# Kernel optimization log

Hardware: AMD Instinct MI355X
Metric: run time of the kernel (lower is better)

Reference implementation:

```python
import jax, jax.numpy as jnp
import numpy as np

N = 50000      # nodes
E = 800000     # edges
F = 128        # num_features == emb_dim
K = 8          # latent factors
d = 16         # emb_dim // K
G = 512        # num graphs
GC = 3         # gc_layers = num_layer - head_layers = 5 - 2
BN_EPS = 1e-5


def setup_inputs() -> dict:
    key = jax.random.key(0)
    ks = jax.random.split(key, 24)
    x = jax.random.normal(ks[0], (N, F), jnp.float32)
    edge_index = jax.random.randint(ks[1], (2, E), 0, N, jnp.int32)
    batch = jnp.sort(jax.random.randint(ks[2], (N,), 0, G, jnp.int32))
    s = 0.05
    inp = {
        'x': x, 'edge_index': edge_index, 'batch': batch, 'num_graphs': G,
        # stacked gc-layer GIN MLP params (all [F,F] since num_features==emb_dim)
        'gc_W1': jax.random.normal(ks[3], (GC, F, F), jnp.float32) * s,
        'gc_b1': jnp.zeros((GC, F), jnp.float32),
        'gc_W2': jax.random.normal(ks[4], (GC, F, F), jnp.float32) * s,
        'gc_b2': jnp.zeros((GC, F), jnp.float32),
        'gc_g': jnp.ones((GC, F), jnp.float32),
        'gc_be': jnp.zeros((GC, F), jnp.float32),
        # disentangled head layer 0 (per factor k): Linear(F,d), Linear(d,d)
        'h0_W1': jax.random.normal(ks[5], (K, F, d), jnp.float32) * s,
        'h0_b1': jnp.zeros((K, d), jnp.float32),
        'h0_W2': jax.random.normal(ks[6], (K, d, d), jnp.float32) * s,
        'h0_b2': jnp.zeros((K, d), jnp.float32),
        'h0_g': jnp.ones((K, d), jnp.float32),
        'h0_be': jnp.zeros((K, d), jnp.float32),
        # disentangled head layer 1: Linear(d,d), Linear(d,d)
        'h1_W1': jax.random.normal(ks[7], (K, d, d), jnp.float32) * s,
        'h1_b1': jnp.zeros((K, d), jnp.float32),
        'h1_W2': jax.random.normal(ks[8], (K, d, d), jnp.float32) * s,
        'h1_b2': jnp.zeros((K, d), jnp.float32),
        'h1_g': jnp.ones((K, d), jnp.float32),
        'h1_be': jnp.zeros((K, d), jnp.float32),
    }
    return inp


def _gin(h, src, dst, W1, b1, W2, b2):
    # GINConv(eps=0): nn(x + sum_{j in N(i)} x_j)
    agg = jax.ops.segment_sum(h[src], dst, num_segments=N)
    z = h + agg
    return jax.nn.relu(z @ W1 + b1) @ W2 + b2


def _bn(z, g, be):
    # BatchNorm1d, training-mode batch statistics over the node axis
    mu = jnp.mean(z, axis=0)
    var = jnp.var(z, axis=0)
    return (z - mu) * jax.lax.rsqrt(var + BN_EPS) * g + be


def reference(x, edge_index, batch, num_graphs,
              gc_W1, gc_b1, gc_W2, gc_b2, gc_g, gc_be,
              h0_W1, h0_b1, h0_W2, h0_b2, h0_g, h0_be,
              h1_W1, h1_b1, h1_W2, h1_b2, h1_g, h1_be):
    src, dst = edge_index[0], edge_index[1]
    # _normal_conv (JK='last', drop_ratio=0, residual off)
    h = x
    for i in range(GC):
        h = _gin(h, src, dst, gc_W1[i], gc_b1[i], gc_W2[i], gc_b2[i])
        h = _bn(h, gc_g[i], gc_be[i])
        if i < GC - 1:
            h = jax.nn.relu(h)
    # _disen_conv: K factor heads, head_layers=2, vmapped over K
    def head(W1a, b1a, W2a, b2a, ga, bea, W1b, b1b, W2b, b2b, gb, beb):
        z = _gin(h, src, dst, W1a, b1a, W2a, b2a)
        z = jax.nn.relu(_bn(z, ga, bea))
        z = _gin(z, src, dst, W1b, b1b, W2b, b2b)
        return _bn(z, gb, beb)
    x_node = jax.vmap(head)(h0_W1, h0_b1, h0_W2, h0_b2, h0_g, h0_be,
                            h1_W1, h1_b1, h1_W2, h1_b2, h1_g, h1_be)  # [K,N,d]
    # global_add_pool per factor
    pool = jax.vmap(lambda z: jax.ops.segment_sum(z, batch, num_segments=num_graphs))
    x_graph = pool(x_node)                        # [K,G,d]
    z_graph = jnp.transpose(x_graph, (1, 0, 2))   # [G,K,d]
    return z_graph
```

## Files before the change

### kernel.cpp

```cpp
#include <hip/hip_runtime.h>

#define NN 50000
#define NE 800000
#define FF 128
#define KF 8
#define DD 16
#define GG 512
#define BN_EPS 1e-5f
#define NB 196
#define KSTR 264
#define BSTR 20

using s8v = __attribute__((ext_vector_type(8))) short;
using f4v = __attribute__((ext_vector_type(4))) float;
using h4v = __attribute__((ext_vector_type(4))) _Float16;
using h8v = __attribute__((ext_vector_type(8))) _Float16;
typedef unsigned int u32;

__device__ __forceinline__ void gload_lds16(const void* g, void* l) {
    __builtin_amdgcn_global_load_lds((const __attribute__((address_space(1))) u32*)g,
                                     (__attribute__((address_space(3))) u32*)l, 16, 0, 0);
}

__global__ void k_deg(const int* __restrict__ dst, int* __restrict__ deg) {
    int e = blockIdx.x * 256 + threadIdx.x;
    if (e < NE) atomicAdd(&deg[dst[e]], 1);
}

__global__ __launch_bounds__(256) void k_bsum(const int* __restrict__ deg, int* __restrict__ bsum) {
    int idx = blockIdx.x * 256 + threadIdx.x;
    int v = (idx < NN) ? deg[idx] : 0;
#pragma unroll
    for (int off = 32; off; off >>= 1) v += __shfl_down(v, off, 64);
    __shared__ int ws[4];
    if ((threadIdx.x & 63) == 0) ws[threadIdx.x >> 6] = v;
    __syncthreads();
    if (threadIdx.x == 0) bsum[blockIdx.x] = ws[0] + ws[1] + ws[2] + ws[3];
}

__global__ __launch_bounds__(256) void k_bscan(const int* __restrict__ bsum, int* __restrict__ boffs) {
    __shared__ int s[256];
    int tid = threadIdx.x;
    int v = (tid < NB) ? bsum[tid] : 0;
    s[tid] = v;
    __syncthreads();
    for (int off = 1; off < 256; off <<= 1) {
        int t = (tid >= off) ? s[tid - off] : 0;
        __syncthreads();
        s[tid] += t;
        __syncthreads();
    }
    if (tid < NB) boffs[tid] = s[tid] - v;
}

__global__ __launch_bounds__(256) void k_offs(const int* __restrict__ deg,
                                              const int* __restrict__ boffs,
                                              int* __restrict__ offs) {
    __shared__ int s[256];
    int tid = threadIdx.x;
    int idx = blockIdx.x * 256 + tid;
    int v = (idx < NN) ? deg[idx] : 0;
    s[tid] = v;
    __syncthreads();
    for (int off = 1; off < 256; off <<= 1) {
        int t = (tid >= off) ? s[tid - off] : 0;
        __syncthreads();
        s[tid] += t;
        __syncthreads();
    }
    int incl = s[tid];
    if (idx < NN) offs[idx] = boffs[blockIdx.x] + incl - v;
    if (idx == NN - 1) offs[NN] = boffs[blockIdx.x] + incl;
}

__global__ void k_fill(const int* __restrict__ src, const int* __restrict__ dst,
                       const int* __restrict__ offs, int* __restrict__ cnt,
                       int* __restrict__ csr) {
    int e = blockIdx.x * 256 + threadIdx.x;
    if (e < NE) {
        int d = dst[e];
        int p = atomicAdd(&cnt[d], 1);
        csr[offs[d] + p] = src[e];
    }
}

__device__ __forceinline__ void bn_coefs(const float* st, const float* g, const float* be,
                                         int lane, float4& a4, float4& b4) {
    const float inv_n = 1.0f / (float)NN;
    float av[4], bv[4];
#pragma unroll
    for (int t = 0; t < 4; t++) {
        int c = lane * 4 + t;
        float mu = st[c] * inv_n;
        float var = st[FF + c] * inv_n - mu * mu;
        float a = g[c] * rsqrtf(var + BN_EPS);
        av[t] = a;
        bv[t] = be[c] - mu * a;
    }
    a4 = make_float4(av[0], av[1], av[2], av[3]);
    b4 = make_float4(bv[0], bv[1], bv[2], bv[3]);
}

__device__ __forceinline__ float4 h2f(h4v h) {
    return make_float4((float)h.x, (float)h.y, (float)h.z, (float)h.w);
}

__global__ __launch_bounds__(256) void k_cvt(const float4* __restrict__ X, h4v* __restrict__ O) {
    int i = blockIdx.x * 256 + threadIdx.x;
    if (i < NN * 32) {
        float4 v = X[i];
        h4v o;
        o.x = (_Float16)v.x; o.y = (_Float16)v.y;
        o.z = (_Float16)v.z; o.w = (_Float16)v.w;
        O[i] = o;
    }
}

__global__ __launch_bounds__(256) void k_wprep(const float* __restrict__ W1,
                                               const float* __restrict__ W2,
                                               unsigned short* __restrict__ out) {
    int idx = blockIdx.x * 256 + threadIdx.x;
    if (idx >= 3 * 2 * 16384) return;
    int l = idx / (2 * 16384);
    int rem = idx % (2 * 16384);
    int mat = rem >> 14;
    int e = rem & 16383;
    int n = e >> 7, k = e & 127;
    const float* W = (mat == 0) ? (W1 + (size_t)l * 16384) : (W2 + (size_t)l * 16384);
    float v = W[k * 128 + n];
    _Float16* o = (_Float16*)out + (size_t)(l * 2 + mat) * 16384;
    o[n * 128 + k] = (_Float16)v;
}

__global__ __launch_bounds__(256) void k_wprep_h0(const float* __restrict__ W1,
                                                  const float* __restrict__ W2,
                                                  unsigned short* __restrict__ out) {
    int idx = blockIdx.x * 256 + threadIdx.x;
    if (idx >= 2 * 16384) return;
    int mat = idx >> 14;
    int e = idx & 16383;
    int n = e >> 7, k = e & 127;
    float v;
    if (mat == 0) {
        v = W1[(n >> 4) * (FF * DD) + k * DD + (n & 15)];
    } else {
        v = ((k >> 4) == (n >> 4)) ? W2[(n >> 4) * 256 + (k & 15) * DD + (n & 15)] : 0.f;
    }
    _Float16* o = (_Float16*)out + (size_t)(6 + mat) * 16384;
    o[n * 128 + k] = (_Float16)v;
}

template <bool BN, bool RELU>
__global__ __launch_bounds__(256) void k_agg(const h4v* __restrict__ X,
                                             const int* __restrict__ offs,
                                             const int* __restrict__ csr,
                                             const float* __restrict__ st,
                                             const float* __restrict__ g,
                                             const float* __restrict__ be,
                                             h4v* __restrict__ Zh) {
    int grp = threadIdx.x >> 5;
    int lane = threadIdx.x & 31;
    int n = blockIdx.x * 8 + grp;

    float4 a4 = make_float4(1.f, 1.f, 1.f, 1.f);
    float4 b4 = make_float4(0.f, 0.f, 0.f, 0.f);
    if (BN) bn_coefs(st, g, be, lane, a4, b4);

    auto apply = [&](float4 v) -> float4 {
        if (BN) {
            v.x = fmaf(v.x, a4.x, b4.x);
            v.y = fmaf(v.y, a4.y, b4.y);
            v.z = fmaf(v.z, a4.z, b4.z);
            v.w = fmaf(v.w, a4.w, b4.w);
        }
        if (RELU) {
            v.x = fmaxf(v.x, 0.f);
            v.y = fmaxf(v.y, 0.f);
            v.z = fmaxf(v.z, 0.f);
            v.w = fmaxf(v.w, 0.f);
        }
        return v;
    };
    auto add4 = [](float4& a, float4 b) {
        a.x += b.x; a.y += b.y; a.z += b.z; a.w += b.w;
    };

    float4 acc = apply(h2f(X[(size_t)n * 32 + lane]));
    int e0 = offs[n], e1 = offs[n + 1];
    int e = e0;
    int s0, s1, s2, s3, s4, s5, s6, s7;
    if (e + 8 <= e1) {
        s0 = csr[e]; s1 = csr[e + 1]; s2 = csr[e + 2]; s3 = csr[e + 3];
        s4 = csr[e + 4]; s5 = csr[e + 5]; s6 = csr[e + 6]; s7 = csr[e + 7];
    }
    while (e + 8 <= e1) {
        h4v r0 = X[(size_t)s0 * 32 + lane];
        h4v r1 = X[(size_t)s1 * 32 + lane];
        h4v r2 = X[(size_t)s2 * 32 + lane];
        h4v r3 = X[(size_t)s3 * 32 + lane];
        h4v r4 = X[(size_t)s4 * 32 + lane];
        h4v r5 = X[(size_t)s5 * 32 + lane];
        h4v r6 = X[(size_t)s6 * 32 + lane];
        h4v r7 = X[(size_t)s7 * 32 + lane];
        e += 8;
        int t0 = csr[e], t1 = csr[e + 1], t2 = csr[e + 2], t3 = csr[e + 3];
        int t4 = csr[e + 4], t5 = csr[e + 5], t6 = csr[e + 6], t7 = csr[e + 7];
        float4 v0 = apply(h2f(r0));
        float4 v1 = apply(h2f(r1));
        float4 v2 = apply(h2f(r2));
        float4 v3 = apply(h2f(r3));
        float4 v4 = apply(h2f(r4));
        float4 v5 = apply(h2f(r5));
        float4 v6 = apply(h2f(r6));
        float4 v7 = apply(h2f(r7));
        add4(v0, v1); add4(v2, v3); add4(v4, v5); add4(v6, v7);
        add4(v0, v2); add4(v4, v6); add4(v0, v4); add4(acc, v0);
        s0 = t0; s1 = t1; s2 = t2; s3 = t3;
        s4 = t4; s5 = t5; s6 = t6; s7 = t7;
    }
    for (; e + 4 <= e1; e += 4) {
        int q0 = csr[e], q1 = csr[e + 1], q2 = csr[e + 2], q3 = csr[e + 3];
        float4 v0 = apply(h2f(X[(size_t)q0 * 32 + lane]));
        float4 v1 = apply(h2f(X[(size_t)q1 * 32 + lane]));
        float4 v2 = apply(h2f(X[(size_t)q2 * 32 + lane]));
        float4 v3 = apply(h2f(X[(size_t)q3 * 32 + lane]));
        add4(v0, v1); add4(v2, v3); add4(v0, v2); add4(acc, v0);
    }
    for (; e < e1; e++) {
        float4 v = apply(h2f(X[(size_t)csr[e] * 32 + lane]));
        add4(acc, v);
    }
    h4v o;
    o.x = (_Float16)acc.x; o.y = (_Float16)acc.y;
    o.z = (_Float16)acc.z; o.w = (_Float16)acc.w;
    Zh[(size_t)n * 32 + lane] = o;
}

__global__ __launch_bounds__(256) void gemm_mfma(const _Float16* __restrict__ A,
                                                 const unsigned short* __restrict__ W1T,
                                                 const unsigned short* __restrict__ W2T,
                                                 const float* __restrict__ b1,
                                                 const float* __restrict__ b2,
                                                 _Float16* __restrict__ C,
                                                 float* __restrict__ stout) {
    __shared__ __align__(16) unsigned short Zs[8192];
    __shared__ __align__(16) unsigned short Wch[8192];
    __shared__ float Sred[1024];
    int tid = threadIdx.x;
    int row0 = blockIdx.x * 64;
    int w = tid >> 6, lane = tid & 63, quad = lane >> 4, lid = lane & 15;

    int wsrc[2], wdst[2];
#pragma unroll
    for (int i = 0; i < 2; i++) {
        int L = (w * 2 + i) * 1024 + lane * 16;
        int npair = L >> 7, cc = L & 127;
        int ccp = cc ^ ((npair & 7) << 4);
        wsrc[i] = (npair * 2 + (ccp >> 6)) * 128 + ((ccp & 63) >> 1);
        wdst[i] = (w * 2 + i) * 1024;
    }

#pragma unroll
    for (int i = 0; i < 4; i++) {
        int L = (w * 4 + i) * 1024 + lane * 16;
        int row = L >> 8, cb = L & 255;
        int cbp = cb ^ ((row & 7) << 4);
        int grow = row0 + row;
        if (grow >= NN) grow = NN - 1;
        gload_lds16((const char*)A + (size_t)grow * 256 + cbp,
                    (char*)Zs + (w * 4 + i) * 1024);
    }
#pragma unroll
    for (int i = 0; i < 2; i++)
        gload_lds16(W1T + wsrc[i], (char*)Wch + wdst[i]);
    __syncthreads();

    int lr = w * 16 + lid;
    int swzr = (lr & 7) << 4;
    int abase = lr * 256;
    int boff[8];
#pragma unroll
    for (int n0 = 0; n0 < 8; n0++) {
        int nn = n0 * 16 + lid;
        int cc = ((nn & 1) << 6) | (quad << 4);
        boff[n0] = (nn >> 1) * 128 + (cc ^ (((nn >> 1) & 7) << 4));
    }

    f4v acc[8];
#pragma unroll
    for (int i = 0; i < 8; i++) acc[i] = 0;

    for (int g = 0; g < 8; ++g) {
        int buf = g & 1;
        if (g < 7) {
            const unsigned short* WT = (g + 1 < 4) ? W1T : W2T;
            int kcn = (g + 1) & 3;
#pragma unroll
            for (int i = 0; i < 2; i++)
                gload_lds16(WT + wsrc[i] + kcn * 32,
                            (char*)Wch + (buf ^ 1) * 8192 + wdst[i]);
        }
        int kc = g & 3;
        int aoff = (kc * 64 + quad * 16) ^ swzr;
        h8v a = *(const h8v*)((const char*)Zs + abase + aoff);
        const char* wb = (const char*)Wch + buf * 8192;
#pragma unroll
        for (int n0 = 0; n0 < 8; n0++) {
            h8v b = *(const h8v*)(wb + boff[n0]);
            acc[n0] = __builtin_amdgcn_mfma_f32_16x16x32_f16(a, b, acc[n0], 0, 0, 0);
        }
        if (g == 3) {
#pragma unroll
            for (int n0 = 0; n0 < 8; n0++) {
                int c = n0 * 16 + lid;
                float bb = b1[c];
#pragma unroll
                for (int rr = 0; rr < 4; rr++) {
                    int zr = w * 16 + quad * 4 + rr;
                    float z = fmaxf(acc[n0][rr] + bb, 0.f);
                    int zb = zr * 256 + ((2 * c) ^ ((zr & 7) << 4));
                    *(_Float16*)((char*)Zs + zb) = (_Float16)z;
                }
                acc[n0] = 0;
            }
        }
        if (g < 7) __syncthreads();
    }

#pragma unroll
    for (int n0 = 0; n0 < 8; n0++) {
        int c = n0 * 16 + lid;
        float bb = b2[c];
        float s = 0.f, q = 0.f;
#pragma unroll
        for (int rr = 0; rr < 4; rr++) {
            int grow = row0 + w * 16 + quad * 4 + rr;
            if (grow < NN) {
                float v = acc[n0][rr] + bb;
                C[(size_t)grow * 128 + c] = (_Float16)v;
                s += v;
                q += v * v;
            }
        }
        s += __shfl_xor(s, 16); s += __shfl_xor(s, 32);
        q += __shfl_xor(q, 16); q += __shfl_xor(q, 32);
        if (quad == 0) {
            Sred[w * 128 + c] = s;
            Sred[512 + w * 128 + c] = q;
        }
    }
    __syncthreads();
    if (tid < 128) {
        float s = Sred[tid] + Sred[128 + tid] + Sred[256 + tid] + Sred[384 + tid];
        float q = Sred[512 + tid] + Sred[640 + tid] + Sred[768 + tid] + Sred[896 + tid];
        atomicAdd(&stout[tid], s);
        atomicAdd(&stout[FF + tid], q);
    }
}

__global__ __launch_bounds__(256) void k_aggbd(const h4v* __restrict__ X,
                                               const int* __restrict__ offs,
                                               const int* __restrict__ csr,
                                               const float* __restrict__ st,
                                               const float* __restrict__ g,
                                               const float* __restrict__ be,
                                               const float* __restrict__ W1,
                                               const float4* __restrict__ b1,
                                               const float* __restrict__ W2,
                                               const float4* __restrict__ b2,
                                               float4* __restrict__ C) {
    __shared__ float As[8][8 * BSTR];
    __shared__ float Ts[8][8 * BSTR];
    __shared__ float Ws1[KF * KSTR];
    __shared__ float Ws2[KF * KSTR];
    int grp = threadIdx.x >> 5, lane = threadIdx.x & 31;
    int n = blockIdx.x * 8 + grp;

    for (int l = threadIdx.x; l < KF * 256; l += 256) {
        int k = l >> 8, r = l & 255;
        Ws1[k * KSTR + r] = W1[l];
        Ws2[k * KSTR + r] = W2[l];
    }

    float4 a4, b4;
    bn_coefs(st, g, be, lane, a4, b4);
    auto apply = [&](float4 v) -> float4 {
        v.x = fmaxf(fmaf(v.x, a4.x, b4.x), 0.f);
        v.y = fmaxf(fmaf(v.y, a4.y, b4.y), 0.f);
        v.z = fmaxf(fmaf(v.z, a4.z, b4.z), 0.f);
        v.w = fmaxf(fmaf(v.w, a4.w, b4.w), 0.f);
        return v;
    };
    auto add4 = [](float4& a, float4 b) {
        a.x += b.x; a.y += b.y; a.z += b.z; a.w += b.w;
    };

    float4 acc = apply(h2f(X[(size_t)n * 32 + lane]));
    int e0 = offs[n], e1 = offs[n + 1];
    int e = e0;
    int s0, s1, s2, s3, s4, s5, s6, s7;
    if (e + 8 <= e1) {
        s0 = csr[e]; s1 = csr[e + 1]; s2 = csr[e + 2]; s3 = csr[e + 3];
        s4 = csr[e + 4]; s5 = csr[e + 5]; s6 = csr[e + 6]; s7 = csr[e + 7];
    }
    while (e + 8 <= e1) {
        h4v r0 = X[(size_t)s0 * 32 + lane];
        h4v r1 = X[(size_t)s1 * 32 + lane];
        h4v r2 = X[(size_t)s2 * 32 + lane];
        h4v r3 = X[(size_t)s3 * 32 + lane];
        h4v r4 = X[(size_t)s4 * 32 + lane];
        h4v r5 = X[(size_t)s5 * 32 + lane];
        h4v r6 = X[(size_t)s6 * 32 + lane];
        h4v r7 = X[(size_t)s7 * 32 + lane];
        e += 8;
        int t0 = csr[e], t1 = csr[e + 1], t2 = csr[e + 2], t3 = csr[e + 3];
        int t4 = csr[e + 4], t5 = csr[e + 5], t6 = csr[e + 6], t7 = csr[e + 7];
        float4 v0 = apply(h2f(r0));
        float4 v1 = apply(h2f(r1));
        float4 v2 = apply(h2f(r2));
        float4 v3 = apply(h2f(r3));
        float4 v4 = apply(h2f(r4));
        float4 v5 = apply(h2f(r5));
        float4 v6 = apply(h2f(r6));
        float4 v7 = apply(h2f(r7));
        add4(v0, v1); add4(v2, v3); add4(v4, v5); add4(v6, v7);
        add4(v0, v2); add4(v4, v6); add4(v0, v4); add4(acc, v0);
        s0 = t0; s1 = t1; s2 = t2; s3 = t3;
        s4 = t4; s5 = t5; s6 = t6; s7 = t7;
    }
    for (; e + 4 <= e1; e += 4) {
        int q0 = csr[e], q1 = csr[e + 1], q2 = csr[e + 2], q3 = csr[e + 3];
        float4 v0 = apply(h2f(X[(size_t)q0 * 32 + lane]));
        float4 v1 = apply(h2f(X[(size_t)q1 * 32 + lane]));
        float4 v2 = apply(h2f(X[(size_t)q2 * 32 + lane]));
        float4 v3 = apply(h2f(X[(size_t)q3 * 32 + lane]));
        add4(v0, v1); add4(v2, v3); add4(v0, v2); add4(acc, v0);
    }
    for (; e < e1; e++) {
        float4 v = apply(h2f(X[(size_t)csr[e] * 32 + lane]));
        add4(acc, v);
    }
    *(float4*)&As[grp][(lane >> 2) * BSTR + (lane & 3) * 4] = acc;
    __syncthreads();

    int k = lane >> 2, jb = (lane & 3) * 4;
    float a[16];
    {
        const float4* As4 = (const float4*)&As[grp][k * BSTR];
        float4 a0 = As4[0], a1 = As4[1], a2 = As4[2], a3 = As4[3];
        a[0] = a0.x; a[1] = a0.y; a[2] = a0.z; a[3] = a0.w;
        a[4] = a1.x; a[5] = a1.y; a[6] = a1.z; a[7] = a1.w;
        a[8] = a2.x; a[9] = a2.y; a[10] = a2.z; a[11] = a2.w;
        a[12] = a3.x; a[13] = a3.y; a[14] = a3.z; a[15] = a3.w;
    }
    const float* wp1 = &Ws1[k * KSTR + jb];
    float4 t = b1[lane];
#pragma unroll
    for (int i = 0; i < 16; i++) {
        float4 wv = *(const float4*)&wp1[i * 16];
        t.x = fmaf(a[i], wv.x, t.x);
        t.y = fmaf(a[i], wv.y, t.y);
        t.z = fmaf(a[i], wv.z, t.z);
        t.w = fmaf(a[i], wv.w, t.w);
    }
    t.x = fmaxf(t.x, 0.f); t.y = fmaxf(t.y, 0.f);
    t.z = fmaxf(t.z, 0.f); t.w = fmaxf(t.w, 0.f);
    *(float4*)&Ts[grp][(lane >> 2) * BSTR + (lane & 3) * 4] = t;
    __syncthreads();

    float b[16];
    {
        const float4* Ts4 = (const float4*)&Ts[grp][k * BSTR];
        float4 a0 = Ts4[0], a1 = Ts4[1], a2 = Ts4[2], a3 = Ts4[3];
        b[0] = a0.x; b[1] = a0.y; b[2] = a0.z; b[3] = a0.w;
        b[4] = a1.x; b[5] = a1.y; b[6] = a1.z; b[7] = a1.w;
        b[8] = a2.x; b[9] = a2.y; b[10] = a2.z; b[11] = a2.w;
        b[12] = a3.x; b[13] = a3.y; b[14] = a3.z; b[15] = a3.w;
    }
    const float* wp2 = &Ws2[k * KSTR + jb];
    float4 acc2 = b2[lane];
#pragma unroll
    for (int i = 0; i < 16; i++) {
        float4 wv = *(const float4*)&wp2[i * 16];
        acc2.x = fmaf(b[i], wv.x, acc2.x);
        acc2.y = fmaf(b[i], wv.y, acc2.y);
        acc2.z = fmaf(b[i], wv.z, acc2.z);
        acc2.w = fmaf(b[i], wv.w, acc2.w);
    }
    C[(size_t)n * 32 + lane] = acc2;
}

__global__ __launch_bounds__(256) void k_stats(const float* __restrict__ X,
                                               float* __restrict__ st, int nrows) {
    int c = threadIdx.x & 127;
    int half = threadIdx.x >> 7;
    int rpb = (nrows + gridDim.x - 1) / gridDim.x;
    int r0 = blockIdx.x * rpb;
    int r1 = min(r0 + rpb, nrows);
    float s = 0.f, sq = 0.f;
    for (int r = r0 + half; r < r1; r += 2) {
        float v = X[(size_t)r * FF + c];
        s += v;
        sq += v * v;
    }
    atomicAdd(&st[c], s);
    atomicAdd(&st[FF + c], sq);
}

__global__ __launch_bounds__(128) void k_pool(const float* __restrict__ X,
                                              const int* __restrict__ batch,
                                              const float* __restrict__ st,
                                              const float* __restrict__ g,
                                              const float* __restrict__ be,
                                              float* __restrict__ out) {
    int c = threadIdx.x;
    const float inv_n = 1.0f / (float)NN;
    float mu = st[c] * inv_n;
    float var = st[FF + c] * inv_n - mu * mu;
    float a = g[c] * rsqrtf(var + BN_EPS);
    float b = be[c] - mu * a;
    int chunk = (NN + gridDim.x - 1) / gridDim.x;
    int r0 = blockIdx.x * chunk;
    int r1 = min(r0 + chunk, NN);
    if (r0 >= r1) return;
    float acc = 0.f;
    int cnt = 0;
    int cur = batch[r0];
    for (int r = r0; r < r1; r++) {
        int bb = batch[r];
        if (bb != cur) {
            atomicAdd(&out[(size_t)cur * FF + c], fmaf(a, acc, b * (float)cnt));
            acc = 0.f;
            cnt = 0;
            cur = bb;
        }
        acc += X[(size_t)r * FF + c];
        cnt++;
    }
    atomicAdd(&out[(size_t)cur * FF + c], fmaf(a, acc, b * (float)cnt));
}

extern "C" void kernel_launch(void* const* d_in, const int* in_sizes, int n_in,
                              void* d_out, int out_size, void* d_ws, size_t ws_size,
                              hipStream_t stream) {
    const float* x = (const float*)d_in[0];
    const int* ei = (const int*)d_in[1];
    const int* src = ei;
    const int* dst = ei + NE;
    const int* batch = (const int*)d_in[2];
    const float* gc_W1 = (const float*)d_in[4];
    const float* gc_b1 = (const float*)d_in[5];
    const float* gc_W2 = (const float*)d_in[6];
    const float* gc_b2 = (const float*)d_in[7];
    const float* gc_g = (const float*)d_in[8];
    const float* gc_be = (const float*)d_in[9];
    const float* h0_W1 = (const float*)d_in[10];
    const float* h0_b1 = (const float*)d_in[11];
    const float* h0_W2 = (const float*)d_in[12];
    const float* h0_b2 = (const float*)d_in[13];
    const float* h0_g = (const float*)d_in[14];
    const float* h0_be = (const float*)d_in[15];
    const float* h1_W1 = (const float*)d_in[16];
    const float* h1_b1 = (const float*)d_in[17];
    const float* h1_W2 = (const float*)d_in[18];
    const float* h1_b2 = (const float*)d_in[19];
    const float* h1_g = (const float*)d_in[20];
    const float* h1_be = (const float*)d_in[21];

    const size_t NF = (size_t)NN * FF;
    float* P0 = (float*)d_ws;
    float* P1 = P0 + NF;
    float* P2 = P1 + NF;
    float* stats = P2 + NF;
    int* deg = (int*)(stats + 5 * 256);
    int* cnt = deg + NN;
    int* offs = cnt + NN;
    int* bsum = offs + (NN + 4);
    int* boffs = bsum + 256;
    int* csr = boffs + 256;
    unsigned short* wbf = (unsigned short*)(csr + NE);

    h4v* Zh = (h4v*)P0;
    h4v* Hbuf = (h4v*)P1;

    hipMemsetAsync(deg, 0, (size_t)2 * NN * sizeof(int), stream);
    hipMemsetAsync(stats, 0, 5 * 256 * sizeof(float), stream);
    hipMemsetAsync(d_out, 0, (size_t)GG * KF * DD * sizeof(float), stream);

    k_deg<<<(NE + 255) / 256, 256, 0, stream>>>(dst, deg);
    k_bsum<<<NB, 256, 0, stream>>>(deg, bsum);
    k_bscan<<<1, 256, 0, stream>>>(bsum, boffs);
    k_offs<<<NB, 256, 0, stream>>>(deg, boffs, offs);
    k_fill<<<(NE + 255) / 256, 256, 0, stream>>>(src, dst, offs, cnt, csr);
    k_wprep<<<(3 * 2 * 16384 + 255) / 256, 256, 0, stream>>>(gc_W1, gc_W2, wbf);
    k_wprep_h0<<<(2 * 16384 + 255) / 256, 256, 0, stream>>>(h0_W1, h0_W2, wbf);
    k_cvt<<<(NN * 32 + 255) / 256, 256, 0, stream>>>((const float4*)x, Hbuf);

    const int agg_grid = NN / 8;
    const int gemm_grid = (NN + 63) / 64;

    k_agg<false, false><<<agg_grid, 256, 0, stream>>>(
        Hbuf, offs, csr, nullptr, nullptr, nullptr, Zh);
    gemm_mfma<<<gemm_grid, 256, 0, stream>>>(
        (const _Float16*)Zh, wbf + 0 * 16384, wbf + 1 * 16384, gc_b1, gc_b2,
        (_Float16*)Hbuf, stats);

    k_agg<true, true><<<agg_grid, 256, 0, stream>>>(
        Hbuf, offs, csr, stats, gc_g, gc_be, Zh);
    gemm_mfma<<<gemm_grid, 256, 0, stream>>>(
        (const _Float16*)Zh, wbf + 2 * 16384, wbf + 3 * 16384, gc_b1 + FF, gc_b2 + FF,
        (_Float16*)Hbuf, stats + 256);

    k_agg<true, true><<<agg_grid, 256, 0, stream>>>(
        Hbuf, offs, csr, stats + 256, gc_g + FF, gc_be + FF, Zh);
    gemm_mfma<<<gemm_grid, 256, 0, stream>>>(
        (const _Float16*)Zh, wbf + 4 * 16384, wbf + 5 * 16384, gc_b1 + 2 * FF, gc_b2 + 2 * FF,
        (_Float16*)Hbuf, stats + 512);

    k_agg<true, false><<<agg_grid, 256, 0, stream>>>(
        Hbuf, offs, csr, stats + 512, gc_g + 2 * FF, gc_be + 2 * FF, Zh);
    gemm_mfma<<<gemm_grid, 256, 0, stream>>>(
        (const _Float16*)Zh, wbf + 6 * 16384, wbf + 7 * 16384, h0_b1, h0_b2,
        (_Float16*)Hbuf, stats + 768);

    k_aggbd<<<agg_grid, 256, 0, stream>>>(
        Hbuf, offs, csr, stats + 768, h0_g, h0_be,
        h1_W1, (const float4*)h1_b1, h1_W2, (const float4*)h1_b2, (float4*)P2);
    k_stats<<<256, 256, 0, stream>>>(P2, stats + 1024, NN);

    k_pool<<<512, 128, 0, stream>>>(P2, batch, stats + 1024, h1_g, h1_be, (float*)d_out);
}
```

Before: 576.0 us.

## Fuse neighbor aggregation into MFMA GEMM kernel, writing aggregated rows to LDS

Merges the CSR gather-sum kernel into the MLP GEMM kernel. Each 64-row block first aggregates its nodes' neighbours directly into the swizzled LDS A-tile, which removes the fp16 intermediate write and read and four kernel launches. Buffers now ping-pong so a layer does not overwrite its own input. For the non-ReLU BN case, the affine transform is applied once after summing, scaled by the neighbour count. The risk is lower parallelism in the gather phase: fewer blocks, and each warp half handles 8 nodes serially, so gather latency hiding may drop while the weight load waits behind it.

```diff
diff --git a/kernel.cpp b/kernel.cpp
--- a/kernel.cpp
+++ b/kernel.cpp
@@ -151,92 +151,12 @@
 }
 
 template <bool BN, bool RELU>
-__global__ __launch_bounds__(256) void k_agg(const h4v* __restrict__ X,
-                                             const int* __restrict__ offs,
-                                             const int* __restrict__ csr,
-                                             const float* __restrict__ st,
-                                             const float* __restrict__ g,
-                                             const float* __restrict__ be,
-                                             h4v* __restrict__ Zh) {
-    int grp = threadIdx.x >> 5;
-    int lane = threadIdx.x & 31;
-    int n = blockIdx.x * 8 + grp;
-
-    float4 a4 = make_float4(1.f, 1.f, 1.f, 1.f);
-    float4 b4 = make_float4(0.f, 0.f, 0.f, 0.f);
-    if (BN) bn_coefs(st, g, be, lane, a4, b4);
-
-    auto apply = [&](float4 v) -> float4 {
-        if (BN) {
-            v.x = fmaf(v.x, a4.x, b4.x);
-            v.y = fmaf(v.y, a4.y, b4.y);
-            v.z = fmaf(v.z, a4.z, b4.z);
-            v.w = fmaf(v.w, a4.w, b4.w);
-        }
-        if (RELU) {
-            v.x = fmaxf(v.x, 0.f);
-            v.y = fmaxf(v.y, 0.f);
-            v.z = fmaxf(v.z, 0.f);
-            v.w = fmaxf(v.w, 0.f);
-        }
-        return v;
-    };
-    auto add4 = [](float4& a, float4 b) {
-        a.x += b.x; a.y += b.y; a.z += b.z; a.w += b.w;
-    };
-
-    float4 acc = apply(h2f(X[(size_t)n * 32 + lane]));
-    int e0 = offs[n], e1 = offs[n + 1];
-    int e = e0;
-    int s0, s1, s2, s3, s4, s5, s6, s7;
-    if (e + 8 <= e1) {
-        s0 = csr[e]; s1 = csr[e + 1]; s2 = csr[e + 2]; s3 = csr[e + 3];
-        s4 = csr[e + 4]; s5 = csr[e + 5]; s6 = csr[e + 6]; s7 = csr[e + 7];
-    }
-    while (e + 8 <= e1) {
-        h4v r0 = X[(size_t)s0 * 32 + lane];
-        h4v r1 = X[(size_t)s1 * 32 + lane];
-        h4v r2 = X[(size_t)s2 * 32 + lane];
-        h4v r3 = X[(size_t)s3 * 32 + lane];
-        h4v r4 = X[(size_t)s4 * 32 + lane];
-        h4v r5 = X[(size_t)s5 * 32 + lane];
-        h4v r6 = X[(size_t)s6 * 32 + lane];
-        h4v r7 = X[(size_t)s7 * 32 + lane];
-        e += 8;
-        int t0 = csr[e], t1 = csr[e + 1], t2 = csr[e + 2], t3 = csr[e + 3];
-        int t4 = csr[e + 4], t5 = csr[e + 5], t6 = csr[e + 6], t7 = csr[e + 7];
-        float4 v0 = apply(h2f(r0));
-        float4 v1 = apply(h2f(r1));
-        float4 v2 = apply(h2f(r2));
-        float4 v3 = apply(h2f(r3));
-        float4 v4 = apply(h2f(r4));
-        float4 v5 = apply(h2f(r5));
-        float4 v6 = apply(h2f(r6));
-        float4 v7 = apply(h2f(r7));
-        add4(v0, v1); add4(v2, v3); add4(v4, v5); add4(v6, v7);
-        add4(v0, v2); add4(v4, v6); add4(v0, v4); add4(acc, v0);
-        s0 = t0; s1 = t1; s2 = t2; s3 = t3;
-        s4 = t4; s5 = t5; s6 = t6; s7 = t7;
-    }
-    for (; e + 4 <= e1; e += 4) {
-        int q0 = csr[e], q1 = csr[e + 1], q2 = csr[e + 2], q3 = csr[e + 3];
-        float4 v0 = apply(h2f(X[(size_t)q0 * 32 + lane]));
-        float4 v1 = apply(h2f(X[(size_t)q1 * 32 + lane]));
-        float4 v2 = apply(h2f(X[(size_t)q2 * 32 + lane]));
-        float4 v3 = apply(h2f(X[(size_t)q3 * 32 + lane]));
-        add4(v0, v1); add4(v2, v3); add4(v0, v2); add4(acc, v0);
-    }
-    for (; e < e1; e++) {
-        float4 v = apply(h2f(X[(size_t)csr[e] * 32 + lane]));
-        add4(acc, v);
-    }
-    h4v o;
-    o.x = (_Float16)acc.x; o.y = (_Float16)acc.y;
-    o.z = (_Float16)acc.z; o.w = (_Float16)acc.w;
-    Zh[(size_t)n * 32 + lane] = o;
-}
-
-__global__ __launch_bounds__(256) void gemm_mfma(const _Float16* __restrict__ A,
+__global__ __launch_bounds__(256) void gagg_mfma(const h4v* __restrict__ X,
+                                                 const int* __restrict__ offs,
+                                                 const int* __restrict__ csr,
+                                                 const float* __restrict__ st,
+                                                 const float* __restrict__ g,
+                                                 const float* __restrict__ be,
                                                  const unsigned short* __restrict__ W1T,
                                                  const unsigned short* __restrict__ W2T,
                                                  const float* __restrict__ b1,
@@ -249,6 +169,7 @@
     int tid = threadIdx.x;
     int row0 = blockIdx.x * 64;
     int w = tid >> 6, lane = tid & 63, quad = lane >> 4, lid = lane & 15;
+    int grp = tid >> 5, l32 = tid & 31;
 
     int wsrc[2], wdst[2];
 #pragma unroll
@@ -259,20 +180,89 @@
         wsrc[i] = (npair * 2 + (ccp >> 6)) * 128 + ((ccp & 63) >> 1);
         wdst[i] = (w * 2 + i) * 1024;
     }
-
-#pragma unroll
-    for (int i = 0; i < 4; i++) {
-        int L = (w * 4 + i) * 1024 + lane * 16;
-        int row = L >> 8, cb = L & 255;
-        int cbp = cb ^ ((row & 7) << 4);
-        int grow = row0 + row;
-        if (grow >= NN) grow = NN - 1;
-        gload_lds16((const char*)A + (size_t)grow * 256 + cbp,
-                    (char*)Zs + (w * 4 + i) * 1024);
-    }
 #pragma unroll
     for (int i = 0; i < 2; i++)
         gload_lds16(W1T + wsrc[i], (char*)Wch + wdst[i]);
+
+    float4 a4 = make_float4(1.f, 1.f, 1.f, 1.f);
+    float4 b4 = make_float4(0.f, 0.f, 0.f, 0.f);
+    if (BN) bn_coefs(st, g, be, l32, a4, b4);
+
+    auto apply = [&](float4 v) -> float4 {
+        if (BN && RELU) {
+            v.x = fmaxf(fmaf(v.x, a4.x, b4.x), 0.f);
+            v.y = fmaxf(fmaf(v.y, a4.y, b4.y), 0.f);
+            v.z = fmaxf(fmaf(v.z, a4.z, b4.z), 0.f);
+            v.w = fmaxf(fmaf(v.w, a4.w, b4.w), 0.f);
+        }
+        return v;
+    };
+    auto add4 = [](float4& a, float4 b) {
+        a.x += b.x; a.y += b.y; a.z += b.z; a.w += b.w;
+    };
+
+    for (int i = 0; i < 8; i++) {
+        int r = grp * 8 + i;
+        int n = row0 + r;
+        int nc = (n < NN) ? n : NN - 1;
+        int e0v = offs[nc], e1v = offs[nc + 1];
+        float4 acc = apply(h2f(X[(size_t)nc * 32 + l32]));
+        int e = e0v;
+        int s0, s1, s2, s3, s4, s5, s6, s7;
+        if (e + 8 <= e1v) {
+            s0 = csr[e]; s1 = csr[e + 1]; s2 = csr[e + 2]; s3 = csr[e + 3];
+            s4 = csr[e + 4]; s5 = csr[e + 5]; s6 = csr[e + 6]; s7 = csr[e + 7];
+        }
+        while (e + 8 <= e1v) {
+            h4v r0 = X[(size_t)s0 * 32 + l32];
+            h4v r1 = X[(size_t)s1 * 32 + l32];
+            h4v r2 = X[(size_t)s2 * 32 + l32];
+            h4v r3 = X[(size_t)s3 * 32 + l32];
+            h4v r4 = X[(size_t)s4 * 32 + l32];
+            h4v r5 = X[(size_t)s5 * 32 + l32];
+            h4v r6 = X[(size_t)s6 * 32 + l32];
+            h4v r7 = X[(size_t)s7 * 32 + l32];
+            e += 8;
+            int t0 = csr[e], t1 = csr[e + 1], t2 = csr[e + 2], t3 = csr[e + 3];
+            int t4 = csr[e + 4], t5 = csr[e + 5], t6 = csr[e + 6], t7 = csr[e + 7];
+            float4 v0 = apply(h2f(r0));
+            float4 v1 = apply(h2f(r1));
+            float4 v2 = apply(h2f(r2));
+            float4 v3 = apply(h2f(r3));
+            float4 v4 = apply(h2f(r4));
+            float4 v5 = apply(h2f(r5));
+            float4 v6 = apply(h2f(r6));
+            float4 v7 = apply(h2f(r7));
+            add4(v0, v1); add4(v2, v3); add4(v4, v5); add4(v6, v7);
+            add4(v0, v2); add4(v4, v6); add4(v0, v4); add4(acc, v0);
+            s0 = t0; s1 = t1; s2 = t2; s3 = t3;
+            s4 = t4; s5 = t5; s6 = t6; s7 = t7;
+        }
+        for (; e + 4 <= e1v; e += 4) {
+            int q0 = csr[e], q1 = csr[e + 1], q2 = csr[e + 2], q3 = csr[e + 3];
+            float4 v0 = apply(h2f(X[(size_t)q0 * 32 + l32]));
+            float4 v1 = apply(h2f(X[(size_t)q1 * 32 + l32]));
+            float4 v2 = apply(h2f(X[(size_t)q2 * 32 + l32]));
+            float4 v3 = apply(h2f(X[(size_t)q3 * 32 + l32]));
+            add4(v0, v1); add4(v2, v3); add4(v0, v2); add4(acc, v0);
+        }
+        for (; e < e1v; e++) {
+            float4 v = apply(h2f(X[(size_t)csr[e] * 32 + l32]));
+            add4(acc, v);
+        }
+        if (BN && !RELU) {
+            float cnt = (float)(e1v - e0v + 1);
+            acc.x = fmaf(acc.x, a4.x, cnt * b4.x);
+            acc.y = fmaf(acc.y, a4.y, cnt * b4.y);
+            acc.z = fmaf(acc.z, a4.z, cnt * b4.z);
+            acc.w = fmaf(acc.w, a4.w, cnt * b4.w);
+        }
+        h4v o;
+        o.x = (_Float16)acc.x; o.y = (_Float16)acc.y;
+        o.z = (_Float16)acc.z; o.w = (_Float16)acc.w;
+        int zb = r * 256 + ((l32 * 8) ^ ((r & 7) << 4));
+        *(h4v*)((char*)Zs + zb) = o;
+    }
     __syncthreads();
 
     int lr = w * 16 + lid;
@@ -290,17 +280,17 @@
 #pragma unroll
     for (int i = 0; i < 8; i++) acc[i] = 0;
 
-    for (int g = 0; g < 8; ++g) {
-        int buf = g & 1;
-        if (g < 7) {
-            const unsigned short* WT = (g + 1 < 4) ? W1T : W2T;
-            int kcn = (g + 1) & 3;
+    for (int gc2 = 0; gc2 < 8; ++gc2) {
+        int buf = gc2 & 1;
+        if (gc2 < 7) {
+            const unsigned short* WT = (gc2 + 1 < 4) ? W1T : W2T;
+            int kcn = (gc2 + 1) & 3;
 #pragma unroll
             for (int i = 0; i < 2; i++)
                 gload_lds16(WT + wsrc[i] + kcn * 32,
                             (char*)Wch + (buf ^ 1) * 8192 + wdst[i]);
         }
-        int kc = g & 3;
+        int kc = gc2 & 3;
         int aoff = (kc * 64 + quad * 16) ^ swzr;
         h8v a = *(const h8v*)((const char*)Zs + abase + aoff);
         const char* wb = (const char*)Wch + buf * 8192;
@@ -309,7 +299,7 @@
             h8v b = *(const h8v*)(wb + boff[n0]);
             acc[n0] = __builtin_amdgcn_mfma_f32_16x16x32_f16(a, b, acc[n0], 0, 0, 0);
         }
-        if (g == 3) {
+        if (gc2 == 3) {
 #pragma unroll
             for (int n0 = 0; n0 < 8; n0++) {
                 int c = n0 * 16 + lid;
@@ -324,7 +314,7 @@
                 acc[n0] = 0;
             }
         }
-        if (g < 7) __syncthreads();
+        if (gc2 < 7) __syncthreads();
     }
 
 #pragma unroll
@@ -580,8 +570,8 @@
     int* csr = boffs + 256;
     unsigned short* wbf = (unsigned short*)(csr + NE);
 
-    h4v* Zh = (h4v*)P0;
-    h4v* Hbuf = (h4v*)P1;
+    h4v* HbufA = (h4v*)P0;
+    h4v* HbufB = (h4v*)P1;
 
     hipMemsetAsync(deg, 0, (size_t)2 * NN * sizeof(int), stream);
     hipMemsetAsync(stats, 0, 5 * 256 * sizeof(float), stream);
@@ -594,37 +584,31 @@
     k_fill<<<(NE + 255) / 256, 256, 0, stream>>>(src, dst, offs, cnt, csr);
     k_wprep<<<(3 * 2 * 16384 + 255) / 256, 256, 0, stream>>>(gc_W1, gc_W2, wbf);
     k_wprep_h0<<<(2 * 16384 + 255) / 256, 256, 0, stream>>>(h0_W1, h0_W2, wbf);
-    k_cvt<<<(NN * 32 + 255) / 256, 256, 0, stream>>>((const float4*)x, Hbuf);
-
+    k_cvt<<<(NN * 32 + 255) / 256, 256, 0, stream>>>((const float4*)x, HbufA);
+
+    const int fus_grid = (NN + 63) / 64;
     const int agg_grid = NN / 8;
-    const int gemm_grid = (NN + 63) / 64;
-
-    k_agg<false, false><<<agg_grid, 256, 0, stream>>>(
-        Hbuf, offs, csr, nullptr, nullptr, nullptr, Zh);
-    gemm_mfma<<<gemm_grid, 256, 0, stream>>>(
-        (const _Float16*)Zh, wbf + 0 * 16384, wbf + 1 * 16384, gc_b1, gc_b2,
-        (_Float16*)Hbuf, stats);
-
-    k_agg<true, true><<<agg_grid, 256, 0, stream>>>(
-        Hbuf, offs, csr, stats, gc_g, gc_be, Zh);
-    gemm_mfma<<<gemm_grid, 256, 0, stream>>>(
-        (const _Float16*)Zh, wbf + 2 * 16384, wbf + 3 * 16384, gc_b1 + FF, gc_b2 + FF,
-        (_Float16*)Hbuf, stats + 256);
-
-    k_agg<true, true><<<agg_grid, 256, 0, stream>>>(
-        Hbuf, offs, csr, stats + 256, gc_g + FF, gc_be + FF, Zh);
-    gemm_mfma<<<gemm_grid, 256, 0, stream>>>(
-        (const _Float16*)Zh, wbf + 4 * 16384, wbf + 5 * 16384, gc_b1 + 2 * FF, gc_b2 + 2 * FF,
-        (_Float16*)Hbuf, stats + 512);
-
-    k_agg<true, false><<<agg_grid, 256, 0, stream>>>(
-        Hbuf, offs, csr, stats + 512, gc_g + 2 * FF, gc_be + 2 * FF, Zh);
-    gemm_mfma<<<gemm_grid, 256, 0, stream>>>(
-        (const _Float16*)Zh, wbf + 6 * 16384, wbf + 7 * 16384, h0_b1, h0_b2,
-        (_Float16*)Hbuf, stats + 768);
+
+    gagg_mfma<false, false><<<fus_grid, 256, 0, stream>>>(
+        HbufA, offs, csr, nullptr, nullptr, nullptr,
+        wbf + 0 * 16384, wbf + 1 * 16384, gc_b1, gc_b2, (_Float16*)HbufB, stats);
+
+    gagg_mfma<true, true><<<fus_grid, 256, 0, stream>>>(
+        HbufB, offs, csr, stats, gc_g, gc_be,
+        wbf + 2 * 16384, wbf + 3 * 16384, gc_b1 + FF, gc_b2 + FF, (_Float16*)HbufA,
+        stats + 256);
+
+    gagg_mfma<true, true><<<fus_grid, 256, 0, stream>>>(
+        HbufA, offs, csr, stats + 256, gc_g + FF, gc_be + FF,
+        wbf + 4 * 16384, wbf + 5 * 16384, gc_b1 + 2 * FF, gc_b2 + 2 * FF, (_Float16*)HbufB,
+        stats + 512);
+
+    gagg_mfma<true, false><<<fus_grid, 256, 0, stream>>>(
+        HbufB, offs, csr, stats + 512, gc_g + 2 * FF, gc_be + 2 * FF,
+        wbf + 6 * 16384, wbf + 7 * 16384, h0_b1, h0_b2, (_Float16*)HbufA, stats + 768);
 
     k_aggbd<<<agg_grid, 256, 0, stream>>>(
-        Hbuf, offs, csr, stats + 768, h0_g, h0_be,
+        HbufA, offs, csr, stats + 768, h0_g, h0_be,
         h1_W1, (const float4*)h1_b1, h1_W2, (const float4*)h1_b2, (float4*)P2);
     k_stats<<<256, 256, 0, stream>>>(P2, stats + 1024, NN);
 
```

New measurement: 644.6 us. 1.12x slower.

## Split aggregation over column slices and edge lanes with shuffle reduction

Applied to the files above, without the earlier changes.

The GIN neighbor aggregation kernel now splits the 128 feature columns into 4 slices across blocks. Within each 32-lane group, 4 sub-groups of 8 lanes each take different edges, and the partial sums are combined with xor shuffles at the end. For BN without ReLU, the affine transform is applied once after summation, scaled by the node's degree count, instead of per neighbor. This aims to expose more memory-level parallelism and finer-grained gathers. The cost is 4x more blocks, repeated csr and offset reads per slice, and narrower 64-byte row segments per gather.

```diff
diff --git a/kernel.cpp b/kernel.cpp
--- a/kernel.cpp
+++ b/kernel.cpp
@@ -158,82 +158,99 @@
                                              const float* __restrict__ g,
                                              const float* __restrict__ be,
                                              h4v* __restrict__ Zh) {
+    int slice = blockIdx.x & 3;
+    int nodeblk = blockIdx.x >> 2;
     int grp = threadIdx.x >> 5;
     int lane = threadIdx.x & 31;
-    int n = blockIdx.x * 8 + grp;
+    int sub = lane >> 3;
+    int li = lane & 7;
+    int n = nodeblk * 8 + grp;
+    int colbase = slice * 8 + li;
 
     float4 a4 = make_float4(1.f, 1.f, 1.f, 1.f);
     float4 b4 = make_float4(0.f, 0.f, 0.f, 0.f);
-    if (BN) bn_coefs(st, g, be, lane, a4, b4);
+    if (BN) {
+        const float inv_n = 1.0f / (float)NN;
+        float av[4], bv[4];
+#pragma unroll
+        for (int t = 0; t < 4; t++) {
+            int c = slice * 32 + li * 4 + t;
+            float mu = st[c] * inv_n;
+            float var = st[FF + c] * inv_n - mu * mu;
+            float a = g[c] * rsqrtf(var + BN_EPS);
+            av[t] = a;
+            bv[t] = be[c] - mu * a;
+        }
+        a4 = make_float4(av[0], av[1], av[2], av[3]);
+        b4 = make_float4(bv[0], bv[1], bv[2], bv[3]);
+    }
 
     auto apply = [&](float4 v) -> float4 {
-        if (BN) {
-            v.x = fmaf(v.x, a4.x, b4.x);
-            v.y = fmaf(v.y, a4.y, b4.y);
-            v.z = fmaf(v.z, a4.z, b4.z);
-            v.w = fmaf(v.w, a4.w, b4.w);
-        }
-        if (RELU) {
-            v.x = fmaxf(v.x, 0.f);
-            v.y = fmaxf(v.y, 0.f);
-            v.z = fmaxf(v.z, 0.f);
-            v.w = fmaxf(v.w, 0.f);
+        if (BN && RELU) {
+            v.x = fmaxf(fmaf(v.x, a4.x, b4.x), 0.f);
+            v.y = fmaxf(fmaf(v.y, a4.y, b4.y), 0.f);
+            v.z = fmaxf(fmaf(v.z, a4.z, b4.z), 0.f);
+            v.w = fmaxf(fmaf(v.w, a4.w, b4.w), 0.f);
         }
         return v;
     };
+
+    float4 acc = make_float4(0.f, 0.f, 0.f, 0.f);
     auto add4 = [](float4& a, float4 b) {
         a.x += b.x; a.y += b.y; a.z += b.z; a.w += b.w;
     };
 
-    float4 acc = apply(h2f(X[(size_t)n * 32 + lane]));
     int e0 = offs[n], e1 = offs[n + 1];
     int e = e0;
-    int s0, s1, s2, s3, s4, s5, s6, s7;
+    int i0, i1;
     if (e + 8 <= e1) {
-        s0 = csr[e]; s1 = csr[e + 1]; s2 = csr[e + 2]; s3 = csr[e + 3];
-        s4 = csr[e + 4]; s5 = csr[e + 5]; s6 = csr[e + 6]; s7 = csr[e + 7];
+        i0 = csr[e + sub];
+        i1 = csr[e + 4 + sub];
     }
     while (e + 8 <= e1) {
-        h4v r0 = X[(size_t)s0 * 32 + lane];
-        h4v r1 = X[(size_t)s1 * 32 + lane];
-        h4v r2 = X[(size_t)s2 * 32 + lane];
-        h4v r3 = X[(size_t)s3 * 32 + lane];
-        h4v r4 = X[(size_t)s4 * 32 + lane];
-        h4v r5 = X[(size_t)s5 * 32 + lane];
-        h4v r6 = X[(size_t)s6 * 32 + lane];
-        h4v r7 = X[(size_t)s7 * 32 + lane];
+        h4v r0 = X[(size_t)i0 * 32 + colbase];
+        h4v r1 = X[(size_t)i1 * 32 + colbase];
         e += 8;
-        int t0 = csr[e], t1 = csr[e + 1], t2 = csr[e + 2], t3 = csr[e + 3];
-        int t4 = csr[e + 4], t5 = csr[e + 5], t6 = csr[e + 6], t7 = csr[e + 7];
-        float4 v0 = apply(h2f(r0));
-        float4 v1 = apply(h2f(r1));
-        float4 v2 = apply(h2f(r2));
-        float4 v3 = apply(h2f(r3));
-        float4 v4 = apply(h2f(r4));
-        float4 v5 = apply(h2f(r5));
-        float4 v6 = apply(h2f(r6));
-        float4 v7 = apply(h2f(r7));
-        add4(v0, v1); add4(v2, v3); add4(v4, v5); add4(v6, v7);
-        add4(v0, v2); add4(v4, v6); add4(v0, v4); add4(acc, v0);
-        s0 = t0; s1 = t1; s2 = t2; s3 = t3;
-        s4 = t4; s5 = t5; s6 = t6; s7 = t7;
-    }
-    for (; e + 4 <= e1; e += 4) {
-        int q0 = csr[e], q1 = csr[e + 1], q2 = csr[e + 2], q3 = csr[e + 3];
-        float4 v0 = apply(h2f(X[(size_t)q0 * 32 + lane]));
-        float4 v1 = apply(h2f(X[(size_t)q1 * 32 + lane]));
-        float4 v2 = apply(h2f(X[(size_t)q2 * 32 + lane]));
-        float4 v3 = apply(h2f(X[(size_t)q3 * 32 + lane]));
-        add4(v0, v1); add4(v2, v3); add4(v0, v2); add4(acc, v0);
-    }
-    for (; e < e1; e++) {
-        float4 v = apply(h2f(X[(size_t)csr[e] * 32 + lane]));
-        add4(acc, v);
-    }
-    h4v o;
-    o.x = (_Float16)acc.x; o.y = (_Float16)acc.y;
-    o.z = (_Float16)acc.z; o.w = (_Float16)acc.w;
-    Zh[(size_t)n * 32 + lane] = o;
+        int t0 = csr[e + sub];
+        int t1 = csr[e + 4 + sub];
+        add4(acc, apply(h2f(r0)));
+        add4(acc, apply(h2f(r1)));
+        i0 = t0; i1 = t1;
+    }
+    for (; e < e1; e += 4) {
+        if (e + sub < e1) {
+            int q = csr[e + sub];
+            add4(acc, apply(h2f(X[(size_t)q * 32 + colbase])));
+        }
+    }
+
+    acc.x += __shfl_xor(acc.x, 8);  acc.y += __shfl_xor(acc.y, 8);
+    acc.z += __shfl_xor(acc.z, 8);  acc.w += __shfl_xor(acc.w, 8);
+    acc.x += __shfl_xor(acc.x, 16); acc.y += __shfl_xor(acc.y, 16);
+    acc.z += __shfl_xor(acc.z, 16); acc.w += __shfl_xor(acc.w, 16);
+
+    if (sub == 0) {
+        float4 self = h2f(X[(size_t)n * 32 + colbase]);
+        float4 fin;
+        if (BN && RELU) {
+            add4(acc, apply(self));
+            fin = acc;
+        } else if (BN) {
+            add4(acc, self);
+            float cnt = (float)(e1 - e0 + 1);
+            fin.x = fmaf(acc.x, a4.x, cnt * b4.x);
+            fin.y = fmaf(acc.y, a4.y, cnt * b4.y);
+            fin.z = fmaf(acc.z, a4.z, cnt * b4.z);
+            fin.w = fmaf(acc.w, a4.w, cnt * b4.w);
+        } else {
+            add4(acc, self);
+            fin = acc;
+        }
+        h4v o;
+        o.x = (_Float16)fin.x; o.y = (_Float16)fin.y;
+        o.z = (_Float16)fin.z; o.w = (_Float16)fin.w;
+        Zh[(size_t)n * 32 + colbase] = o;
+    }
 }
 
 __global__ __launch_bounds__(256) void gemm_mfma(const _Float16* __restrict__ A,
@@ -596,7 +613,8 @@
     k_wprep_h0<<<(2 * 16384 + 255) / 256, 256, 0, stream>>>(h0_W1, h0_W2, wbf);
     k_cvt<<<(NN * 32 + 255) / 256, 256, 0, stream>>>((const float4*)x, Hbuf);
 
-    const int agg_grid = NN / 8;
+    const int agg_grid = (NN / 8) * 4;
+    const int bd_grid = NN / 8;
     const int gemm_grid = (NN + 63) / 64;
 
     k_agg<false, false><<<agg_grid, 256, 0, stream>>>(
@@ -623,7 +641,7 @@
         (const _Float16*)Zh, wbf + 6 * 16384, wbf + 7 * 16384, h0_b1, h0_b2,
         (_Float16*)Hbuf, stats + 768);
 
-    k_aggbd<<<agg_grid, 256, 0, stream>>>(
+    k_aggbd<<<bd_grid, 256, 0, stream>>>(
         Hbuf, offs, csr, stats + 768, h0_g, h0_be,
         h1_W1, (const float4*)h1_b1, h1_W2, (const float4*)h1_b2, (float4*)P2);
     k_stats<<<256, 256, 0, stream>>>(P2, stats + 1024, NN);
```

New measurement: 686.0 us. 1.19x slower.
